# Kernel optimization log

Hardware: AMD Instinct MI355X
Metric: run time of the kernel (lower is better)

The kernel has to match this reference:

```python
import jax, jax.numpy as jnp
import numpy as np

NUM_HEADS = 16


def setup_inputs() -> dict:
    key = jax.random.key(0)
    ks = jax.random.split(key, 6)
    B, N, L, C = 2, 1024, 4096, 1024
    x_obj = jax.random.normal(ks[0], (B, N, C), dtype=jnp.float32)
    x_ctx = jax.random.normal(ks[1], (B, L, C), dtype=jnp.float32)
    s = 1.0 / np.sqrt(C)
    Wq = jax.random.normal(ks[2], (C, C), dtype=jnp.float32) * s
    Wkv = jax.random.normal(ks[3], (C, 2 * C), dtype=jnp.float32) * s
    Wproj = jax.random.normal(ks[4], (C, C), dtype=jnp.float32) * s
    bproj = jax.random.normal(ks[5], (C,), dtype=jnp.float32) * 0.01
    return {"x_obj": x_obj, "x_ctx": x_ctx, "Wq": Wq, "Wkv": Wkv,
            "Wproj": Wproj, "bproj": bproj}


def _split_heads(t, H):
    # [B, T, C] -> [B, H, T, d]
    B, T, C = t.shape
    return t.reshape(B, T, H, C // H).transpose(0, 2, 1, 3)


def reference(x_obj, x_ctx, Wq, Wkv, Wproj, bproj):
    B, N, C = x_obj.shape
    H = NUM_HEADS
    d = C // H
    scale = d ** -0.5

    q = _split_heads(x_obj @ Wq, H)                      # [B,H,N,d]

    kv_o = x_obj @ Wkv                                   # [B,N,2C] -> (2,H,d) split
    k_obj = _split_heads(kv_o[..., :C], H)               # [B,H,N,d]
    v_obj = _split_heads(kv_o[..., C:], H)

    kv_c = x_ctx @ Wkv                                   # [B,L,2C]
    k_ctx = _split_heads(kv_c[..., :C], H)               # [B,H,L,d]
    v_ctx = _split_heads(kv_c[..., C:], H)

    k = jnp.concatenate([k_obj, k_ctx], axis=2)          # [B,H,N+L,d]
    v = jnp.concatenate([v_obj, v_ctx], axis=2)

    attn = jnp.einsum('bhnd,bhmd->bhnm', q, k) * scale   # [B,H,N,N+L]
    attn = jax.nn.softmax(attn, axis=-1)
    out = jnp.einsum('bhnm,bhmd->bhnd', attn, v)         # [B,H,N,d]
    out = out.transpose(0, 2, 1, 3).reshape(B, N, C)
    return out @ Wproj + bproj
```

## Files before the change

kernel.cpp:

```cpp
#include <hip/hip_runtime.h>
#include <stdint.h>

typedef unsigned short u16;
typedef unsigned int   u32;
typedef __attribute__((ext_vector_type(8))) short bf16x8;
typedef __attribute__((ext_vector_type(4))) float f32x4;

__device__ __forceinline__ u16 f2bf(float f) {
    union { float f; u32 u; } v; v.f = f;
    return (u16)((v.u + 0x7FFFu + ((v.u >> 16) & 1u)) >> 16);
}
__device__ __forceinline__ float bf2f(u16 h) {
    union { u32 u; float f; } v; v.u = ((u32)h) << 16; return v.f;
}
__device__ __forceinline__ u32 fbits(float f) {
    union { float f; u32 u; } v; v.f = f; return v.u;
}

__device__ __forceinline__ void async16(const u16* g, u16* l) {
    typedef __attribute__((address_space(1))) const u32 gq;
    typedef __attribute__((address_space(3))) u32 lq;
    __builtin_amdgcn_global_load_lds((gq*)g, (lq*)l, 16, 0, 0);
}

__global__ void cvt_all_k(const float* __restrict__ xo, const float* __restrict__ xc,
                          u16* __restrict__ Xc,
                          const float* __restrict__ Wq, const float* __restrict__ Wkv,
                          const float* __restrict__ Wp,
                          u16* __restrict__ Wqt, u16* __restrict__ Wkt,
                          u16* __restrict__ Wpt)
{
    __shared__ __align__(16) u16 Ts[64][72];
    int id = blockIdx.x, t = threadIdx.x;
    if (id < 10240) {
        int row = id, cid = t * 4;
        int b = row >= 5120, s = row - b * 5120;
        const float* src = (s < 1024)
            ? xo + ((size_t)(b * 1024 + s)) * 1024 + cid
            : xc + ((size_t)(b * 4096 + s - 1024)) * 1024 + cid;
        float4 f = *(const float4*)src;
        union { u16 a[4]; uint2 v; } p;
        p.a[0]=f2bf(f.x); p.a[1]=f2bf(f.y); p.a[2]=f2bf(f.z); p.a[3]=f2bf(f.w);
        *(uint2*)(Xc + (size_t)row * 1024 + cid) = p.v;
        return;
    }
    int wid = id - 10240;
    const float* W; u16* Wt; int N, tile;
    if (wid < 256)      { W = Wq;  Wt = Wqt; N = 1024; tile = wid; }
    else if (wid < 768) { W = Wkv; Wt = Wkt; N = 2048; tile = wid - 256; }
    else                { W = Wp;  Wt = Wpt; N = 1024; tile = wid - 768; }
    int nt = N >> 6;
    int n0 = (tile % nt) * 64, k0 = (tile / nt) * 64;
    int lr = t >> 2, lc = (t & 3) * 16;
    const float* src = W + (size_t)(k0 + lr) * N + n0 + lc;
    union { u16 a[8]; uint4 v; } p0, p1;
    float4 f0 = *(const float4*)(src),      f1 = *(const float4*)(src + 4);
    float4 f2 = *(const float4*)(src + 8),  f3 = *(const float4*)(src + 12);
    p0.a[0]=f2bf(f0.x); p0.a[1]=f2bf(f0.y); p0.a[2]=f2bf(f0.z); p0.a[3]=f2bf(f0.w);
    p0.a[4]=f2bf(f1.x); p0.a[5]=f2bf(f1.y); p0.a[6]=f2bf(f1.z); p0.a[7]=f2bf(f1.w);
    p1.a[0]=f2bf(f2.x); p1.a[1]=f2bf(f2.y); p1.a[2]=f2bf(f2.z); p1.a[3]=f2bf(f2.w);
    p1.a[4]=f2bf(f3.x); p1.a[5]=f2bf(f3.y); p1.a[6]=f2bf(f3.z); p1.a[7]=f2bf(f3.w);
    *(uint4*)&Ts[lr][lc]     = p0.v;
    *(uint4*)&Ts[lr][lc + 8] = p1.v;
    __syncthreads();
    union { u16 a[8]; uint4 v; } q0, q1;
#pragma unroll
    for (int j = 0; j < 8; ++j) q0.a[j] = Ts[lc + j][lr];
#pragma unroll
    for (int j = 0; j < 8; ++j) q1.a[j] = Ts[lc + 8 + j][lr];
    u16* dst = Wt + (size_t)(n0 + lr) * 1024 + k0 + lc;
    *(uint4*)dst       = q0.v;
    *(uint4*)(dst + 8) = q1.v;
}

__global__ __launch_bounds__(256, 3)
void gemm_qkv(const u16* __restrict__ A, const u16* __restrict__ Wqt,
              const u16* __restrict__ Wkt, u16* __restrict__ q,
              u16* __restrict__ Kh, u16* __restrict__ Vh)
{
    __shared__ __align__(16) u16 smem[17408];
    u16* As = smem;
    u16* Bs = smem + 4096;

    const int t = threadIdx.x, w = t >> 6;
    const int lane = t & 63, quad = lane >> 4, l16 = lane & 15;
    const int id = blockIdx.x;
    const bool qm = id >= 1280;
    int m0, n0; const u16* Bt;
    if (qm) { int t2 = id - 1280; m0 = (t2 >> 3) * 128; n0 = (t2 & 7) * 128; Bt = Wqt; }
    else    { m0 = (id >> 4) * 128; n0 = (id & 15) * 128; Bt = Wkt; }
    const int wr = (w >> 1) * 64, wc = (w & 1) * 64;

    const int sr0 = w * 32 + (lane >> 2), sr1 = sr0 + 16;
    const int cg  = (lane & 3) ^ ((lane >> 4) & 3);
    u16* abase = As + w * 1024;
    u16* bbase = Bs + w * 1024;

    const u16 *ar0, *ar1;
    {
        int g0 = m0 + sr0, g1 = m0 + sr1;
        if (qm) {
            ar0 = A + ((size_t)(g0 >> 10) * 5120 + (g0 & 1023)) * 1024;
            ar1 = A + ((size_t)(g1 >> 10) * 5120 + (g1 & 1023)) * 1024;
        } else {
            ar0 = A + (size_t)g0 * 1024;
            ar1 = A + (size_t)g1 * 1024;
        }
        ar0 += cg * 8; ar1 += cg * 8;
    }
    const u16* br0 = Bt + (size_t)(n0 + sr0) * 1024 + cg * 8;
    const u16* br1 = Bt + (size_t)(n0 + sr1) * 1024 + cg * 8;

    f32x4 acc[4][4] = {};
    const int sel = (quad ^ (l16 >> 2)) * 8;

    for (int k0 = 0; k0 < 1024; k0 += 32) {
        async16(ar0 + k0, abase);
        async16(ar1 + k0, abase + 512);
        async16(br0 + k0, bbase);
        async16(br1 + k0, bbase + 512);
        __syncthreads();

        bf16x8 av[4], bv[4];
#pragma unroll
        for (int i = 0; i < 4; ++i)
            av[i] = *(const bf16x8*)&As[(wr + i * 16 + l16) * 32 + sel];
#pragma unroll
        for (int j = 0; j < 4; ++j)
            bv[j] = *(const bf16x8*)&Bs[(wc + j * 16 + l16) * 32 + sel];
#pragma unroll
        for (int i = 0; i < 4; ++i)
#pragma unroll
            for (int j = 0; j < 4; ++j)
                acc[i][j] = __builtin_amdgcn_mfma_f32_16x16x32_bf16(av[i], bv[j], acc[i][j], 0, 0, 0);
        __syncthreads();
    }

    if (qm) {
#pragma unroll
        for (int j = 0; j < 4; ++j) {
            int col = n0 + wc + j * 16 + l16;
#pragma unroll
            for (int i = 0; i < 4; ++i) {
                int rowb = m0 + wr + i * 16 + quad * 4;
#pragma unroll
                for (int r = 0; r < 4; ++r)
                    q[(size_t)(rowb + r) * 1024 + col] = f2bf(acc[i][j][r]);
            }
        }
    } else if (n0 < 1024) {
#pragma unroll
        for (int j = 0; j < 4; ++j) {
            int col = n0 + wc + j * 16 + l16;
#pragma unroll
            for (int i = 0; i < 4; ++i) {
                int rowb = m0 + wr + i * 16 + quad * 4;
                int b = rowb >= 5120;
                int key = rowb - b * 5120;
                int bh = b * 16 + (col >> 6), d = col & 63;
                u16* dst = Kh + ((size_t)bh * 5120 + key) * 64 + d;
#pragma unroll
                for (int r = 0; r < 4; ++r) dst[r * 64] = f2bf(acc[i][j][r]);
            }
        }
    } else {
        u16* Tv = smem;
#pragma unroll
        for (int j = 0; j < 4; ++j) {
            int d2 = wc + j * 16 + l16;
#pragma unroll
            for (int i = 0; i < 4; ++i) {
                int kl = wr + i * 16 + quad * 4;
                union { u16 a[4]; uint2 v; } pk;
#pragma unroll
                for (int r = 0; r < 4; ++r) pk.a[r] = f2bf(acc[i][j][r]);
                *(uint2*)&Tv[d2 * 136 + kl] = pk.v;
            }
        }
        __syncthreads();
        int b = m0 >= 5120;
        int keyb = m0 - b * 5120;
        int hb = (n0 - 1024) >> 6;
#pragma unroll
        for (int p = 0; p < 8; ++p) {
            int idx = p * 256 + t;
            int d2 = idx >> 4, k0c = (idx & 15) * 8;
            uint4 vv = *(const uint4*)&Tv[d2 * 136 + k0c];
            int bh = b * 16 + hb + (d2 >> 6), d = d2 & 63;
            *(uint4*)(Vh + ((size_t)bh * 64 + d) * 5120 + keyb + k0c) = vv;
        }
    }
}

__global__ __launch_bounds__(256, 2)
void gemm_proj(const u16* __restrict__ A, const u16* __restrict__ Bt,
               const float* __restrict__ bias, float* __restrict__ Cf)
{
    __shared__ __align__(16) u16 As[128 * 32];
    __shared__ __align__(16) u16 Bs[64 * 32];

    const int t = threadIdx.x, w = t >> 6;
    const int lane = t & 63, quad = lane >> 4, l16 = lane & 15;
    const int m0 = blockIdx.y * 128, n0 = blockIdx.x * 64;
    const int wr = w * 32;

    const int sr0 = w * 32 + (lane >> 2), sr1 = sr0 + 16;
    const int cg  = (lane & 3) ^ ((lane >> 4) & 3);
    u16* abase = As + w * 1024;
    u16* bbase = Bs + w * 512;

    const u16* ar0 = A + (size_t)(m0 + sr0) * 1024 + cg * 8;
    const u16* ar1 = A + (size_t)(m0 + sr1) * 1024 + cg * 8;
    const u16* br0 = Bt + (size_t)(n0 + w * 16 + (lane >> 2)) * 1024 + cg * 8;

    f32x4 acc[2][4] = {};
    const int sel = (quad ^ (l16 >> 2)) * 8;

    for (int k0 = 0; k0 < 1024; k0 += 32) {
        async16(ar0 + k0, abase);
        async16(ar1 + k0, abase + 512);
        async16(br0 + k0, bbase);
        __syncthreads();

        bf16x8 av[2], bv[4];
#pragma unroll
        for (int i = 0; i < 2; ++i)
            av[i] = *(const bf16x8*)&As[(wr + i * 16 + l16) * 32 + sel];
#pragma unroll
        for (int j = 0; j < 4; ++j)
            bv[j] = *(const bf16x8*)&Bs[(j * 16 + l16) * 32 + sel];
#pragma unroll
        for (int i = 0; i < 2; ++i)
#pragma unroll
            for (int j = 0; j < 4; ++j)
                acc[i][j] = __builtin_amdgcn_mfma_f32_16x16x32_bf16(av[i], bv[j], acc[i][j], 0, 0, 0);
        __syncthreads();
    }

#pragma unroll
    for (int j = 0; j < 4; ++j) {
        int col = n0 + j * 16 + l16;
        float bvl = bias[col];
#pragma unroll
        for (int i = 0; i < 2; ++i) {
            int rowb = m0 + wr + i * 16 + quad * 4;
#pragma unroll
            for (int r = 0; r < 4; ++r)
                Cf[(size_t)(rowb + r) * 1024 + col] = acc[i][j][r] + bvl;
        }
    }
}

__global__ __launch_bounds__(256, 4)
void attn_k(const u16* __restrict__ Q, const u16* __restrict__ Kh,
            const u16* __restrict__ Vh, u16* __restrict__ Op,
            float* __restrict__ Lp)
{
    __shared__ __align__(16) u16 Ks[4096];
    __shared__ __align__(16) u16 Vt[4096];
    __shared__ __align__(16) u16 Ps[8192];

    const int tid  = threadIdx.x;
    const int wave = tid >> 6, lane = tid & 63;
    const int quad = lane >> 4, l16 = lane & 15;
    const int bx = blockIdx.x;
    const int part = bx & 3, qt = (bx >> 2) & 7, h = (bx >> 5) & 15, b = bx >> 9;
    const int bh = b * 16 + h;

    const int qrow0 = b * 1024 + qt * 128 + wave * 32;
    const u16* qbase = Q + (size_t)qrow0 * 1024 + h * 64;

    bf16x8 aq[2][2];
#pragma unroll
    for (int rt = 0; rt < 2; ++rt) {
        aq[rt][0] = *(const bf16x8*)(qbase + (size_t)(rt * 16 + l16) * 1024 +      quad * 8);
        aq[rt][1] = *(const bf16x8*)(qbase + (size_t)(rt * 16 + l16) * 1024 + 32 + quad * 8);
    }

    f32x4 o[2][4] = {};
    f32x4 lv[2] = {};

    const u16* kbase = Kh + (size_t)bh * 5120 * 64;
    const u16* vbase = Vh + (size_t)bh * 64 * 5120;
    const int srow = tid >> 2;
    const int scg  = (tid & 3) * 2;
    const int m7   = srow & 7;
    const int l7   = l16 & 7;
    u16* kdst0 = Ks + srow * 64 + ((scg ^ m7) * 8);
    u16* kdst1 = Ks + srow * 64 + (((scg + 1) ^ m7) * 8);
    u16* vdst0 = Vt + srow * 64 + ((scg ^ m7) * 8);
    u16* vdst1 = Vt + srow * 64 + (((scg + 1) ^ m7) * 8);
    u16* psw   = Ps + wave * 2048;
    const int m_beg = part * 1280;
    const float SC = 0.180336880f;

    for (int c = 0; c < 20; ++c) {
        const int m0 = m_beg + c * 64;
        {
            const u16* ks = kbase + (size_t)(m0 + srow) * 64 + scg * 8;
            *(uint4*)kdst0 = *(const uint4*)(ks);
            *(uint4*)kdst1 = *(const uint4*)(ks + 8);
        }
        {
            const u16* vs = vbase + (size_t)srow * 5120 + m0 + (tid & 3) * 4;
            uint2 g0 = *(const uint2*)(vs);
            uint2 g1 = *(const uint2*)(vs + 16);
            uint2 g2 = *(const uint2*)(vs + 32);
            uint2 g3 = *(const uint2*)(vs + 48);
            uint4 o0, o1;
            o0.x = __builtin_amdgcn_perm(g1.x, g0.x, 0x05040100u);
            o0.y = __builtin_amdgcn_perm(g3.x, g2.x, 0x05040100u);
            o0.z = __builtin_amdgcn_perm(g1.x, g0.x, 0x07060302u);
            o0.w = __builtin_amdgcn_perm(g3.x, g2.x, 0x07060302u);
            o1.x = __builtin_amdgcn_perm(g1.y, g0.y, 0x05040100u);
            o1.y = __builtin_amdgcn_perm(g3.y, g2.y, 0x05040100u);
            o1.z = __builtin_amdgcn_perm(g1.y, g0.y, 0x07060302u);
            o1.w = __builtin_amdgcn_perm(g3.y, g2.y, 0x07060302u);
            *(uint4*)vdst0 = o0;
            *(uint4*)vdst1 = o1;
        }
        __syncthreads();

        f32x4 s[2][4] = {};
#pragma unroll
        for (int nt = 0; nt < 4; ++nt) {
            const u16* krow = Ks + (nt * 16 + l16) * 64;
            bf16x8 kb0 = *(const bf16x8*)(krow + ((quad     ^ l7) * 8));
            bf16x8 kb1 = *(const bf16x8*)(krow + (((4+quad) ^ l7) * 8));
#pragma unroll
            for (int rt = 0; rt < 2; ++rt) {
                s[rt][nt] = __builtin_amdgcn_mfma_f32_16x16x32_bf16(aq[rt][0], kb0, s[rt][nt], 0, 0, 0);
                s[rt][nt] = __builtin_amdgcn_mfma_f32_16x16x32_bf16(aq[rt][1], kb1, s[rt][nt], 0, 0, 0);
            }
        }

#pragma unroll
        for (int rt = 0; rt < 2; ++rt)
#pragma unroll
            for (int r = 0; r < 4; ++r) {
                float e0 = exp2f(s[rt][0][r] * SC);
                float e1 = exp2f(s[rt][1][r] * SC);
                float e2 = exp2f(s[rt][2][r] * SC);
                float e3 = exp2f(s[rt][3][r] * SC);
                lv[rt][r] += (e0 + e1) + (e2 + e3);
                uint2 pw;
                pw.x = __builtin_amdgcn_perm(fbits(e1), fbits(e0), 0x07060302u);
                pw.y = __builtin_amdgcn_perm(fbits(e3), fbits(e2), 0x07060302u);
                int qr = quad * 4 + r;
                *(uint2*)(psw + (rt * 16 + qr) * 64 +
                          (((l16 >> 1) ^ (qr & 7)) * 8) + (l16 & 1) * 4) = pw;
            }

        asm volatile("s_waitcnt lgkmcnt(0)" ::: "memory");

        bf16x8 pf[2][2];
#pragma unroll
        for (int rt = 0; rt < 2; ++rt) {
            const u16* prow = psw + (rt * 16 + l16) * 64;
            pf[rt][0] = *(const bf16x8*)(prow + ((quad     ^ l7) * 8));
            pf[rt][1] = *(const bf16x8*)(prow + (((4+quad) ^ l7) * 8));
        }

#pragma unroll
        for (int dt = 0; dt < 4; ++dt) {
            const u16* vrow = Vt + (dt * 16 + l16) * 64;
            bf16x8 v0 = *(const bf16x8*)(vrow + ((quad     ^ l7) * 8));
            bf16x8 v1 = *(const bf16x8*)(vrow + (((4+quad) ^ l7) * 8));
#pragma unroll
            for (int rt = 0; rt < 2; ++rt) {
                o[rt][dt] = __builtin_amdgcn_mfma_f32_16x16x32_bf16(pf[rt][0], v0, o[rt][dt], 0, 0, 0);
                o[rt][dt] = __builtin_amdgcn_mfma_f32_16x16x32_bf16(pf[rt][1], v1, o[rt][dt], 0, 0, 0);
            }
        }
        __syncthreads();
    }

    float lsum[2][4];
#pragma unroll
    for (int rt = 0; rt < 2; ++rt)
#pragma unroll
        for (int r = 0; r < 4; ++r) {
            float x = lv[rt][r];
#pragma unroll
            for (int off = 8; off >= 1; off >>= 1)
                x += __shfl_xor(x, off, 64);
            lsum[rt][r] = x;
        }

    const int Rb = bh * 1024 + qt * 128 + wave * 32;
    u16* obase = Op + ((size_t)part << 21);
#pragma unroll
    for (int rt = 0; rt < 2; ++rt)
#pragma unroll
        for (int dt = 0; dt < 4; ++dt)
#pragma unroll
            for (int r = 0; r < 4; ++r) {
                int R = Rb + rt * 16 + quad * 4 + r;
                obase[(size_t)R * 64 + dt * 16 + l16] = f2bf(o[rt][dt][r]);
            }
    if (l16 == 0) {
#pragma unroll
        for (int rt = 0; rt < 2; ++rt)
#pragma unroll
            for (int r = 0; r < 4; ++r)
                Lp[part * 32768 + Rb + rt * 16 + quad * 4 + r] = lsum[rt][r];
    }
}

__global__ void comb_k(const u16* __restrict__ Op, const float* __restrict__ Lp,
                       u16* __restrict__ ao)
{
    int t = blockIdx.x * 256 + threadIdx.x;
    int R = t >> 4, dg = (t & 15) * 4;
    float l = Lp[R] + Lp[32768 + R] + Lp[65536 + R] + Lp[98304 + R];
    float a[4] = {0.f, 0.f, 0.f, 0.f};
#pragma unroll
    for (int p = 0; p < 4; ++p) {
        union { u16 a[4]; uint2 v; } w;
        w.v = *(const uint2*)(Op + ((size_t)p << 21) + (size_t)R * 64 + dg);
#pragma unroll
        for (int j = 0; j < 4; ++j) a[j] += bf2f(w.a[j]);
    }
    float inv = 1.f / l;
    int bh = R >> 10, n = R & 1023, b = bh >> 4, h = bh & 15;
    union { u16 a[4]; uint2 v; } out;
#pragma unroll
    for (int j = 0; j < 4; ++j) out.a[j] = f2bf(a[j] * inv);
    *(uint2*)(ao + (size_t)(b * 1024 + n) * 1024 + h * 64 + dg) = out.v;
}

extern "C" void kernel_launch(void* const* d_in, const int* in_sizes, int n_in,
                              void* d_out, int out_size, void* d_ws, size_t ws_size,
                              hipStream_t stream)
{
    const float* x_obj = (const float*)d_in[0];
    const float* x_ctx = (const float*)d_in[1];
    const float* Wq    = (const float*)d_in[2];
    const float* Wkv   = (const float*)d_in[3];
    const float* Wproj = (const float*)d_in[4];
    const float* bproj = (const float*)d_in[5];
    float* out = (float*)d_out;

    u16* Xc  = (u16*)d_ws;
    u16* ao  = Xc;
    u16* Op  = Xc + (size_t)2097152;
    u16* Wqt = Xc  + (size_t)10485760;
    u16* Wkt = Wqt + (size_t)1048576;
    u16* Wpt = Wkt + (size_t)2097152;
    u16* q   = Wpt + (size_t)1048576;
    u16* Kh  = q   + (size_t)2097152;
    u16* Vh  = Kh  + (size_t)10485760;
    float* Lp = (float*)(Vh + (size_t)10485760);

    dim3 blk(256);
    cvt_all_k<<<dim3(11264), blk, 0, stream>>>(x_obj, x_ctx, Xc,
                                               Wq, Wkv, Wproj, Wqt, Wkt, Wpt);
    gemm_qkv<<<dim3(1408), blk, 0, stream>>>(Xc, Wqt, Wkt, q, Kh, Vh);
    attn_k<<<dim3(1024), blk, 0, stream>>>(q, Kh, Vh, Op, Lp);
    comb_k<<<dim3(2048), blk, 0, stream>>>(Op, Lp, ao);
    gemm_proj<<<dim3(16, 16), blk, 0, stream>>>(ao, Wpt, bproj, out);
}
```

Baseline: 261.6 us.

## Fold softmax scale into Q, compute row sums via MFMA, coalesce K stores

After: 269.5 us. +3.0%, slower.

```diff
diff --git a/kernel.cpp b/kernel.cpp
--- a/kernel.cpp
+++ b/kernel.cpp
@@ -73,7 +73,7 @@
     *(uint4*)(dst + 8) = q1.v;
 }
 
-__global__ __launch_bounds__(256, 3)
+__global__ __launch_bounds__(256, 2)
 void gemm_qkv(const u16* __restrict__ A, const u16* __restrict__ Wqt,
               const u16* __restrict__ Wkt, u16* __restrict__ q,
               u16* __restrict__ Kh, u16* __restrict__ Vh)
@@ -137,6 +137,7 @@
     }
 
     if (qm) {
+        const float SC = 0.180336880f;
 #pragma unroll
         for (int j = 0; j < 4; ++j) {
             int col = n0 + wc + j * 16 + l16;
@@ -145,47 +146,46 @@
                 int rowb = m0 + wr + i * 16 + quad * 4;
 #pragma unroll
                 for (int r = 0; r < 4; ++r)
-                    q[(size_t)(rowb + r) * 1024 + col] = f2bf(acc[i][j][r]);
+                    q[(size_t)(rowb + r) * 1024 + col] = f2bf(acc[i][j][r] * SC);
             }
         }
-    } else if (n0 < 1024) {
-#pragma unroll
-        for (int j = 0; j < 4; ++j) {
-            int col = n0 + wc + j * 16 + l16;
-#pragma unroll
-            for (int i = 0; i < 4; ++i) {
-                int rowb = m0 + wr + i * 16 + quad * 4;
-                int b = rowb >= 5120;
-                int key = rowb - b * 5120;
-                int bh = b * 16 + (col >> 6), d = col & 63;
-                u16* dst = Kh + ((size_t)bh * 5120 + key) * 64 + d;
-#pragma unroll
-                for (int r = 0; r < 4; ++r) dst[r * 64] = f2bf(acc[i][j][r]);
-            }
+        return;
+    }
+    u16* T = smem;
+#pragma unroll
+    for (int j = 0; j < 4; ++j) {
+        int col = wc + j * 16 + l16;
+#pragma unroll
+        for (int i = 0; i < 4; ++i) {
+            int kl = wr + i * 16 + quad * 4;
+            union { u16 a[4]; uint2 v; } pk;
+#pragma unroll
+            for (int r = 0; r < 4; ++r) pk.a[r] = f2bf(acc[i][j][r]);
+            *(uint2*)&T[col * 136 + kl] = pk.v;
+        }
+    }
+    __syncthreads();
+    int b = m0 >= 5120;
+    int keyb = m0 - b * 5120;
+    if (n0 < 1024) {
+        int hb = n0 >> 6;
+#pragma unroll
+        for (int p = 0; p < 8; ++p) {
+            int idx = p * 256 + t;
+            int key = idx >> 4, cseg = (idx & 15) * 8;
+            union { u16 a[8]; uint4 v; } g;
+#pragma unroll
+            for (int j = 0; j < 8; ++j) g.a[j] = T[(cseg + j) * 136 + key];
+            int bh = b * 16 + hb + (cseg >> 6), d = cseg & 63;
+            *(uint4*)(Kh + ((size_t)bh * 5120 + keyb + key) * 64 + d) = g.v;
         }
     } else {
-        u16* Tv = smem;
-#pragma unroll
-        for (int j = 0; j < 4; ++j) {
-            int d2 = wc + j * 16 + l16;
-#pragma unroll
-            for (int i = 0; i < 4; ++i) {
-                int kl = wr + i * 16 + quad * 4;
-                union { u16 a[4]; uint2 v; } pk;
-#pragma unroll
-                for (int r = 0; r < 4; ++r) pk.a[r] = f2bf(acc[i][j][r]);
-                *(uint2*)&Tv[d2 * 136 + kl] = pk.v;
-            }
-        }
-        __syncthreads();
-        int b = m0 >= 5120;
-        int keyb = m0 - b * 5120;
         int hb = (n0 - 1024) >> 6;
 #pragma unroll
         for (int p = 0; p < 8; ++p) {
             int idx = p * 256 + t;
             int d2 = idx >> 4, k0c = (idx & 15) * 8;
-            uint4 vv = *(const uint4*)&Tv[d2 * 136 + k0c];
+            uint4 vv = *(const uint4*)&T[d2 * 136 + k0c];
             int bh = b * 16 + hb + (d2 >> 6), d = d2 & 63;
             *(uint4*)(Vh + ((size_t)bh * 64 + d) * 5120 + keyb + k0c) = vv;
         }
@@ -277,8 +277,12 @@
         aq[rt][1] = *(const bf16x8*)(qbase + (size_t)(rt * 16 + l16) * 1024 + 32 + quad * 8);
     }
 
+    union { u32 u[4]; bf16x8 v; } onesf;
+#pragma unroll
+    for (int i = 0; i < 4; ++i) onesf.u[i] = 0x3F803F80u;
+
     f32x4 o[2][4] = {};
-    f32x4 lv[2] = {};
+    f32x4 lacc[2] = {};
 
     const u16* kbase = Kh + (size_t)bh * 5120 * 64;
     const u16* vbase = Vh + (size_t)bh * 64 * 5120;
@@ -292,7 +296,6 @@
     u16* vdst1 = Vt + srow * 64 + (((scg + 1) ^ m7) * 8);
     u16* psw   = Ps + wave * 2048;
     const int m_beg = part * 1280;
-    const float SC = 0.180336880f;
 
     for (int c = 0; c < 20; ++c) {
         const int m0 = m_beg + c * 64;
@@ -338,11 +341,10 @@
         for (int rt = 0; rt < 2; ++rt)
 #pragma unroll
             for (int r = 0; r < 4; ++r) {
-                float e0 = exp2f(s[rt][0][r] * SC);
-                float e1 = exp2f(s[rt][1][r] * SC);
-                float e2 = exp2f(s[rt][2][r] * SC);
-                float e3 = exp2f(s[rt][3][r] * SC);
-                lv[rt][r] += (e0 + e1) + (e2 + e3);
+                float e0 = exp2f(s[rt][0][r]);
+                float e1 = exp2f(s[rt][1][r]);
+                float e2 = exp2f(s[rt][2][r]);
+                float e3 = exp2f(s[rt][3][r]);
                 uint2 pw;
                 pw.x = __builtin_amdgcn_perm(fbits(e1), fbits(e0), 0x07060302u);
                 pw.y = __builtin_amdgcn_perm(fbits(e3), fbits(e2), 0x07060302u);
@@ -362,6 +364,12 @@
         }
 
 #pragma unroll
+        for (int rt = 0; rt < 2; ++rt) {
+            lacc[rt] = __builtin_amdgcn_mfma_f32_16x16x32_bf16(pf[rt][0], onesf.v, lacc[rt], 0, 0, 0);
+            lacc[rt] = __builtin_amdgcn_mfma_f32_16x16x32_bf16(pf[rt][1], onesf.v, lacc[rt], 0, 0, 0);
+        }
+
+#pragma unroll
         for (int dt = 0; dt < 4; ++dt) {
             const u16* vrow = Vt + (dt * 16 + l16) * 64;
             bf16x8 v0 = *(const bf16x8*)(vrow + ((quad     ^ l7) * 8));
@@ -374,18 +382,6 @@
         }
         __syncthreads();
     }
-
-    float lsum[2][4];
-#pragma unroll
-    for (int rt = 0; rt < 2; ++rt)
-#pragma unroll
-        for (int r = 0; r < 4; ++r) {
-            float x = lv[rt][r];
-#pragma unroll
-            for (int off = 8; off >= 1; off >>= 1)
-                x += __shfl_xor(x, off, 64);
-            lsum[rt][r] = x;
-        }
 
     const int Rb = bh * 1024 + qt * 128 + wave * 32;
     u16* obase = Op + ((size_t)part << 21);
@@ -403,7 +399,7 @@
         for (int rt = 0; rt < 2; ++rt)
 #pragma unroll
             for (int r = 0; r < 4; ++r)
-                Lp[part * 32768 + Rb + rt * 16 + quad * 4 + r] = lsum[rt][r];
+                Lp[part * 32768 + Rb + rt * 16 + quad * 4 + r] = lacc[rt][r];
     }
 }
 
```
